# Optimization experiments

Measured on AMD Instinct MI355X. Metric: run time of the kernel, lower is better.

## Reference

```python
import jax, jax.numpy as jnp
import numpy as np

N_NODES = 100_000
N_EDGES = 3_200_000
N_FEAT = 128
HIDDEN = 16
OUT = 2
N_GRAPHS = 64


def setup_inputs() -> dict:
    key = jax.random.key(0)
    ks = jax.random.split(key, 12)
    x = jax.random.normal(ks[0], (N_NODES, N_FEAT), dtype=jnp.float32)
    edge_index = jax.random.randint(ks[1], (2, N_EDGES), 0, N_NODES, dtype=jnp.int64)
    batch_idx = jnp.sort(jax.random.randint(ks[2], (N_NODES,), 0, N_GRAPHS, dtype=jnp.int64))

    def glorot(k, shape):
        s = jnp.sqrt(6.0 / (shape[0] + shape[1])).astype(jnp.float32)
        return jax.random.uniform(k, shape, jnp.float32, -1.0, 1.0) * s

    return {
        "x": x, "edge_index": edge_index, "batch_idx": batch_idx,
        "W0": glorot(ks[3], (N_FEAT, HIDDEN)), "b0": jnp.zeros((HIDDEN,), jnp.float32),
        "a0": jnp.full((1,), 0.25, jnp.float32),  # PReLU default weight
        "W1": glorot(ks[4], (HIDDEN, HIDDEN)), "b1": jnp.zeros((HIDDEN,), jnp.float32),
        "a1": jnp.full((1,), 0.25, jnp.float32),
        "W2": glorot(ks[5], (HIDDEN, HIDDEN)), "b2": jnp.zeros((HIDDEN,), jnp.float32),
        "a2": jnp.full((1,), 0.25, jnp.float32),
        "W3": glorot(ks[6], (HIDDEN, OUT)), "b3": jnp.zeros((OUT,), jnp.float32),
    }


def _prelu(x, a):
    return jnp.where(x > 0, x, a * x)


def _gcn_conv(x, W, b, src, dst, norm, n):
    # PyG GCNConv: linear transform, then normalized gather-scatter aggregation, then bias
    h = x @ W                                   # [N, out]
    msg = h[src] * norm[:, None]                # gather + per-edge scale
    out = jax.ops.segment_sum(msg, dst, num_segments=n)  # scatter-add into targets
    return out + b


def reference(x, edge_index, batch_idx, W0, b0, a0, W1, b1, a1, W2, b2, a2, W3, b3):
    n = x.shape[0]
    loop = jnp.arange(n, dtype=edge_index.dtype)
    src = jnp.concatenate([edge_index[0], loop])  # add self loops
    dst = jnp.concatenate([edge_index[1], loop])
    # symmetric degree normalization deg^-1/2 (deg over targets, all edge weights = 1)
    deg = jax.ops.segment_sum(jnp.ones_like(dst, dtype=x.dtype), dst, num_segments=n)
    dinv = jnp.where(deg > 0, jax.lax.rsqrt(deg), 0.0)
    norm = dinv[src] * dinv[dst]

    h = _prelu(_gcn_conv(x, W0, b0, src, dst, norm, n), a0)
    h = _prelu(_gcn_conv(h, W1, b1, src, dst, norm, n), a1)
    h = _prelu(_gcn_conv(h, W2, b2, src, dst, norm, n), a2)
    h = _gcn_conv(h, W3, b3, src, dst, norm, n)

    # global_mean_pool over graph ids
    sums = jax.ops.segment_sum(h, batch_idx, num_segments=N_GRAPHS)
    cnts = jax.ops.segment_sum(jnp.ones((n,), h.dtype), batch_idx, num_segments=N_GRAPHS)
    return sums / jnp.maximum(cnts, 1.0)[:, None]
```

## Files before the change

### kernel.cpp

```cpp
#include <hip/hip_runtime.h>


#define NN 100000
#define NE 3200000
#define NF 128
#define NH 16
#define NO 2
#define NG 64
#define NBLK 391
#define BN 256
#define NBUK 391
#define CHUNK 4096
#define NBLKA 782
#define CAP2 10240


__device__ __forceinline__ float ldf(const void* p, int i, int f32) {
  if (f32) return ((const float*)p)[i];
  unsigned int u = ((const unsigned short*)p)[i];
  return __uint_as_float(u << 16);
}
__device__ __forceinline__ int ldi(const void* p, int i, int i64) {
  if (i64) return (int)((const long long*)p)[i];
  return ((const int*)p)[i];
}
__device__ __forceinline__ void stf(void* p, int i, float v, int f32) {
  if (f32) {
    ((float*)p)[i] = v;
  } else {
    unsigned int w = __float_as_uint(v);
    unsigned int r = (w + 0x7fffu + ((w >> 16) & 1u)) >> 16;
    ((unsigned short*)p)[i] = (unsigned short)r;
  }
}
__device__ __forceinline__ float bf16lo(unsigned int u) { return __uint_as_float(u << 16); }
__device__ __forceinline__ float bf16hi(unsigned int u) { return __uint_as_float(u & 0xffff0000u); }
__device__ __forceinline__ unsigned int packbf(float x, float y) {
  unsigned int a = __float_as_uint(x);
  a = (a + 0x7fffu + ((a >> 16) & 1u)) >> 16;
  unsigned int b = __float_as_uint(y);
  b = (b + 0x7fffu + ((b >> 16) & 1u)) & 0xffff0000u;
  return a | b;
}
__device__ __forceinline__ int okf(float v) { return (v == v) && (fabsf(v) < 1e30f); }
__device__ __forceinline__ void nflag(int* diag, int bad, int bit) {
  if (__any(bad)) {
    if ((threadIdx.x & 63) == 0) atomicOr(diag + 2, 1 << bit);
  }
}
__device__ __forceinline__ int clampi(int v, int hi) {
  return (unsigned)v < (unsigned)hi ? v : 0;
}


__global__ __launch_bounds__(64) void k_sniff(const void* x, const void* ei, int* diag) {
  int lane = threadIdx.x;
  unsigned int xv = ((const unsigned int*)x)[lane];
  unsigned int e = (xv >> 7) & 0xffu;
  int hit = (e >= 116u && e <= 133u);
  int hits = __popcll(__ballot(hit));
  unsigned int ev = ((const unsigned int*)ei)[2 * lane + 1];
  int nzc = __popcll(__ballot(ev != 0u));
  if (lane == 0) {
    diag[0] = (hits < 32) ? 1 : 0;
    diag[1] = (nzc == 0) ? 1 : 0;
  }
}


__global__ __launch_bounds__(256) void k_count(const void* ei, const int* __restrict__ diag,
                                               int* __restrict__ matrix) {
  __shared__ int lh[NBUK];
  int tid = threadIdx.x, blk = blockIdx.x;
  for (int b = tid; b < NBUK; b += 256) lh[b] = 0;
  __syncthreads();
  int i64 = diag[1];
  int base = blk * CHUNK;
  int n = NE - base; n = n > CHUNK ? CHUNK : n;
  for (int i = tid; i < n; i += 256) {
    int d = clampi(ldi(ei, NE + base + i, i64), NN);
    atomicAdd(&lh[d >> 8], 1);
  }
  __syncthreads();
  for (int b = tid; b < NBUK; b += 256) matrix[blk * NBUK + b] = lh[b];
}

__global__ __launch_bounds__(256) void k_rowscan(int* __restrict__ matrix, int* __restrict__ bucket_start) {
  __shared__ int s[1024];
  int tid = threadIdx.x, b = blockIdx.x;
#pragma unroll
  for (int k = 0; k < 4; ++k) {
    int i = tid + 256 * k;
    s[i] = (i < NBLKA) ? matrix[i * NBUK + b] : 0;
  }
  __syncthreads();
  for (int off = 1; off < 1024; off <<= 1) {
    int v[4];
#pragma unroll
    for (int k = 0; k < 4; ++k) { int i = tid + 256 * k; v[k] = (i >= off) ? s[i - off] : 0; }
    __syncthreads();
#pragma unroll
    for (int k = 0; k < 4; ++k) s[tid + 256 * k] += v[k];
    __syncthreads();
  }
#pragma unroll
  for (int k = 0; k < 4; ++k) {
    int i = tid + 256 * k;
    if (i < NBLKA) matrix[i * NBUK + b] = (i > 0) ? s[i - 1] : 0;
  }
  if (tid == 0) bucket_start[b] = s[1023];
}

__global__ __launch_bounds__(512) void k_sscan(int* __restrict__ bucket_start, int* __restrict__ rowstart) {
  __shared__ int s[512];
  int tid = threadIdx.x;
  int v = (tid < NBUK) ? bucket_start[tid] : 0;
  s[tid] = v;
  __syncthreads();
  for (int off = 1; off < 512; off <<= 1) {
    int t = (tid >= off) ? s[tid - off] : 0;
    __syncthreads();
    s[tid] += t;
    __syncthreads();
  }
  if (tid < NBUK) bucket_start[tid] = s[tid] - v;
  if (tid == 511) bucket_start[NBUK] = s[511];
  if (tid == 0) rowstart[NN] = NE;
}

__global__ __launch_bounds__(256) void k_bscatter(const void* ei, const int* __restrict__ diag,
                                                  const int* __restrict__ matrix,
                                                  const int* __restrict__ bucket_start,
                                                  int* __restrict__ ents) {
  __shared__ int ssrc[CHUNK];
  __shared__ int sdst[CHUNK];
  __shared__ int spkt[CHUNK];
  __shared__ int gpos[CHUNK];
  __shared__ int lhist[512];
  __shared__ int lcur[NBUK];
  __shared__ int goff[NBUK];
  int tid = threadIdx.x, blk = blockIdx.x;
  lhist[tid] = 0; lhist[tid + 256] = 0;
  __syncthreads();
  int i64 = diag[1];
  int base = blk * CHUNK;
  int n = NE - base; n = n > CHUNK ? CHUNK : n;
  for (int i = tid; i < n; i += 256) {
    int sv = clampi(ldi(ei, base + i, i64), NN);
    int dv = clampi(ldi(ei, NE + base + i, i64), NN);
    ssrc[i] = sv; sdst[i] = dv;
    atomicAdd(&lhist[dv >> 8], 1);
  }
  __syncthreads();
  for (int off = 1; off < 512; off <<= 1) {
    int v0 = (tid >= off) ? lhist[tid - off] : 0;
    int v1 = lhist[tid + 256 - off];
    __syncthreads();
    lhist[tid] += v0;
    lhist[tid + 256] += v1;
    __syncthreads();
  }
  for (int b = tid; b < NBUK; b += 256) {
    int excl = (b > 0) ? lhist[b - 1] : 0;
    lcur[b] = excl;
    goff[b] = bucket_start[b] + matrix[blk * NBUK + b] - excl;
  }
  __syncthreads();
  for (int i = tid; i < n; i += 256) {
    int dv = sdst[i], b = dv >> 8;
    int r = atomicAdd(&lcur[b], 1);
    spkt[r] = ((dv & 255) << 17) | ssrc[i];
    gpos[r] = goff[b] + r;
  }
  __syncthreads();
  for (int i = tid; i < n; i += 256) ents[gpos[i]] = spkt[i];
}

__global__ __launch_bounds__(256) void k_bsort(int* __restrict__ ents, const int* __restrict__ bucket_start,
                                               int* __restrict__ rowstart, float* __restrict__ dinv,
                                               int* __restrict__ diag) {
  __shared__ int ent[CAP2];
  __shared__ int lh[BN];
  __shared__ int lcur[BN];
  int tid = threadIdx.x, b = blockIdx.x;
  int bs = bucket_start[b], be = bucket_start[b + 1];
  int n = be - bs;
  if (n > CAP2) { n = CAP2; if (tid == 0) atomicOr(diag + 2, 1 << 9); }
  for (int i = tid; i < n; i += 256) ent[i] = ents[bs + i];
  lh[tid] = 0;
  __syncthreads();
  for (int i = tid; i < n; i += 256) atomicAdd(&lh[ent[i] >> 17], 1);
  __syncthreads();
  int c = lh[tid];
  for (int off = 1; off < 256; off <<= 1) {
    int v = (tid >= off) ? lh[tid - off] : 0;
    __syncthreads();
    lh[tid] += v;
    __syncthreads();
  }
  int excl = lh[tid] - c;
  lcur[tid] = excl;
  int node = (b << 8) + tid;
  if (node < NN) {
    rowstart[node] = bs + excl;
    dinv[node] = rsqrtf((float)(c + 1));
  }
  __syncthreads();
  for (int i = tid; i < n; i += 256) {
    int e = ent[i];
    int r = atomicAdd(&lcur[e >> 17], 1);
    ents[bs + r] = e & 0x1FFFF;
  }
}


__global__ __launch_bounds__(256) void k_t0(const void* __restrict__ x, const void* __restrict__ W0,
                                            const float* __restrict__ dinv,
                                            int* __restrict__ diag, unsigned int* __restrict__ out) {
  __shared__ float ws[NF * NH];
  __shared__ float xs[16 * 129];
  int tid = threadIdx.x;
  int f32 = diag[0];
  int node0 = blockIdx.x * 16;
#pragma unroll
  for (int r = 0; r < 8; ++r) ws[tid + 256 * r] = ldf(W0, tid + 256 * r, f32);
#pragma unroll
  for (int r = 0; r < 8; ++r) {
    int idx = tid + 256 * r;
    int row = idx >> 7, col = idx & 127;
    xs[row * 129 + col] = ldf(x, (node0 + row) * NF + col, f32);
  }
  __syncthreads();
  int nl = tid >> 4, f = tid & 15;
  float acc = 0.f;
#pragma unroll 4
  for (int k = 0; k < NF; ++k) acc += xs[nl * 129 + k] * ws[k * NH + f];
  acc *= dinv[node0 + nl];
  float other = __shfl_xor(acc, 1);
  if ((f & 1) == 0) out[(node0 + nl) * 8 + (f >> 1)] = packbf(acc, other);
  nflag(diag, !okf(acc), 0);
}


__global__ __launch_bounds__(256) void k_aggT(const unsigned int* __restrict__ hin,
                                              const int* __restrict__ srcs,
                                              const int* __restrict__ rowstart,
                                              const float* __restrict__ dinv,
                                              const void* __restrict__ b, const void* __restrict__ a,
                                              const void* __restrict__ Wn,
                                              int* __restrict__ diag, int bit,
                                              unsigned int* __restrict__ hout) {
  __shared__ float ws[NH * NH];
  int tid = threadIdx.x;
  int f32 = diag[0];
  ws[tid] = ldf(Wn, tid, f32);
  __syncthreads();
  int gid = blockIdx.x * 256 + tid;
  int node = gid >> 3, p = gid & 7;
  unsigned int self = hin[node * 8 + p];
  float acc0 = bf16lo(self), acc1 = bf16hi(self);
  int e0 = rowstart[node], e1 = rowstart[node + 1];
  int e = e0;
  for (; e + 4 <= e1; e += 4) {
    int s0 = srcs[e], s1 = srcs[e + 1], s2 = srcs[e + 2], s3 = srcs[e + 3];
    unsigned int v0 = hin[s0 * 8 + p];
    unsigned int v1 = hin[s1 * 8 + p];
    unsigned int v2 = hin[s2 * 8 + p];
    unsigned int v3 = hin[s3 * 8 + p];
    acc0 += bf16lo(v0) + bf16lo(v1) + bf16lo(v2) + bf16lo(v3);
    acc1 += bf16hi(v0) + bf16hi(v1) + bf16hi(v2) + bf16hi(v3);
  }
  for (; e < e1; ++e) {
    unsigned int v = hin[srcs[e] * 8 + p];
    acc0 += bf16lo(v);
    acc1 += bf16hi(v);
  }
  float dv = dinv[node];
  float av = ldf(a, 0, f32);
  float p0 = dv * acc0 + ldf(b, 2 * p, f32);
  float p1 = dv * acc1 + ldf(b, 2 * p + 1, f32);
  p0 = p0 > 0.f ? p0 : av * p0;
  p1 = p1 > 0.f ? p1 : av * p1;
  float t0 = 0.f, t1 = 0.f;
#pragma unroll
  for (int j = 0; j < 8; ++j) {
    float qa = __shfl(p0, j, 8);
    float qb = __shfl(p1, j, 8);
    t0 += qa * ws[(2 * j) * NH + 2 * p]     + qb * ws[(2 * j + 1) * NH + 2 * p];
    t1 += qa * ws[(2 * j) * NH + 2 * p + 1] + qb * ws[(2 * j + 1) * NH + 2 * p + 1];
  }
  t0 *= dv;
  t1 *= dv;
  hout[node * 8 + p] = packbf(t0, t1);
  nflag(diag, !okf(t0) || !okf(t1), bit);
}

__global__ __launch_bounds__(256) void k_aggT3(const unsigned int* __restrict__ hin,
                                               const int* __restrict__ srcs,
                                               const int* __restrict__ rowstart,
                                               const float* __restrict__ dinv,
                                               const void* __restrict__ b, const void* __restrict__ a,
                                               const void* __restrict__ W3,
                                               int* __restrict__ diag, float2* __restrict__ hout) {
  __shared__ float ws[NH * NO];
  int tid = threadIdx.x;
  int f32 = diag[0];
  if (tid < NH * NO) ws[tid] = ldf(W3, tid, f32);
  __syncthreads();
  int gid = blockIdx.x * 256 + tid;
  int node = gid >> 3, p = gid & 7;
  unsigned int self = hin[node * 8 + p];
  float acc0 = bf16lo(self), acc1 = bf16hi(self);
  int e0 = rowstart[node], e1 = rowstart[node + 1];
  int e = e0;
  for (; e + 4 <= e1; e += 4) {
    int s0 = srcs[e], s1 = srcs[e + 1], s2 = srcs[e + 2], s3 = srcs[e + 3];
    unsigned int v0 = hin[s0 * 8 + p];
    unsigned int v1 = hin[s1 * 8 + p];
    unsigned int v2 = hin[s2 * 8 + p];
    unsigned int v3 = hin[s3 * 8 + p];
    acc0 += bf16lo(v0) + bf16lo(v1) + bf16lo(v2) + bf16lo(v3);
    acc1 += bf16hi(v0) + bf16hi(v1) + bf16hi(v2) + bf16hi(v3);
  }
  for (; e < e1; ++e) {
    unsigned int v = hin[srcs[e] * 8 + p];
    acc0 += bf16lo(v);
    acc1 += bf16hi(v);
  }
  float dv = dinv[node];
  float av = ldf(a, 0, f32);
  float p0 = dv * acc0 + ldf(b, 2 * p, f32);
  float p1 = dv * acc1 + ldf(b, 2 * p + 1, f32);
  p0 = p0 > 0.f ? p0 : av * p0;
  p1 = p1 > 0.f ? p1 : av * p1;
  float u0 = p0 * ws[(2 * p) * NO] + p1 * ws[(2 * p + 1) * NO];
  float u1 = p0 * ws[(2 * p) * NO + 1] + p1 * ws[(2 * p + 1) * NO + 1];
#pragma unroll
  for (int off = 1; off < 8; off <<= 1) {
    u0 += __shfl_xor(u0, off, 8);
    u1 += __shfl_xor(u1, off, 8);
  }
  if (p == 0) hout[node] = make_float2(dv * u0, dv * u1);
  nflag(diag, !okf(u0) || !okf(u1), 6);
}

__global__ __launch_bounds__(256) void k_agg2(const float2* __restrict__ tin,
                                              const int* __restrict__ srcs,
                                              const int* __restrict__ rowstart,
                                              const float* __restrict__ dinv,
                                              const void* __restrict__ b3,
                                              int* __restrict__ diag, float2* __restrict__ out) {
  int node = blockIdx.x * 256 + threadIdx.x;
  if (node >= NN) return;
  int f32 = diag[0];
  float2 t = tin[node];
  float a0 = t.x, a1 = t.y;
  int e0 = rowstart[node], e1 = rowstart[node + 1];
  int e = e0;
  for (; e + 4 <= e1; e += 4) {
    int s0 = srcs[e], s1 = srcs[e + 1], s2 = srcs[e + 2], s3 = srcs[e + 3];
    float2 h0 = tin[s0], h1 = tin[s1], h2 = tin[s2], h3 = tin[s3];
    a0 += h0.x + h1.x + h2.x + h3.x;
    a1 += h0.y + h1.y + h2.y + h3.y;
  }
  for (; e < e1; ++e) {
    float2 hv = tin[srcs[e]];
    a0 += hv.x;
    a1 += hv.y;
  }
  float dv = dinv[node];
  a0 = dv * a0 + ldf(b3, 0, f32);
  a1 = dv * a1 + ldf(b3, 1, f32);
  out[node] = make_float2(a0, a1);
  nflag(diag, !okf(a0) || !okf(a1), 7);
}


__global__ __launch_bounds__(256) void k_pool(const float2* __restrict__ h, const void* __restrict__ batch,
                                              const int* __restrict__ diag, float* __restrict__ pool) {
  __shared__ float ssum[NG * NO];
  __shared__ float scnt[NG];
  int tid = threadIdx.x;
  if (tid < NG * NO) ssum[tid] = 0.f;
  if (tid < NG) scnt[tid] = 0.f;
  __syncthreads();
  int i = blockIdx.x * 256 + tid;
  if (i < NN) {
    int i64 = diag[1];
    int g = ldi(batch, i, i64);
    g = (unsigned)g < NG ? g : 0;
    float2 v = h[i];
    atomicAdd(&ssum[g * 2], v.x);
    atomicAdd(&ssum[g * 2 + 1], v.y);
    atomicAdd(&scnt[g], 1.f);
  }
  __syncthreads();
  if (tid < NG * NO && ssum[tid] != 0.f) atomicAdd(&pool[tid], ssum[tid]);
  if (tid < NG && scnt[tid] != 0.f) atomicAdd(&pool[NG * NO + tid], scnt[tid]);
}

__global__ __launch_bounds__(128) void k_final(const float* __restrict__ pool,
                                               const int* __restrict__ diag, void* __restrict__ out) {
  int i = threadIdx.x;
  int f32 = diag[0], i64 = diag[1], stg = diag[2];
  float c = pool[NG * NO + (i >> 1)];
  c = c > 1.f ? c : 1.f;
  float v = pool[i] / c;
  if (stg != 0 || !okf(v)) {
    int stage = stg ? __ffs(stg) : 15;
    v = 1024.0f + stage * 64.0f + f32 * 16.0f + i64 * 8.0f;
  }
  stf(out, i, v, f32);
}

__global__ __launch_bounds__(128) void k_diag_ws(void* out, float v) {
  unsigned int w = __float_as_uint(v);
  ((unsigned short*)out)[threadIdx.x] = (unsigned short)(w >> 16);
}


extern "C" void kernel_launch(void* const* d_in, const int* in_sizes, int n_in,
                              void* d_out, int out_size, void* d_ws, size_t ws_size,
                              hipStream_t stream) {
  const void* x  = d_in[0];
  const void* ei = d_in[1];
  const void* batch = d_in[2];
  const void* W0 = d_in[3];
  const void* b0 = d_in[4];
  const void* a0 = d_in[5];
  const void* W1 = d_in[6];
  const void* b1 = d_in[7];
  const void* a1 = d_in[8];
  const void* W2 = d_in[9];
  const void* b2 = d_in[10];
  const void* a2 = d_in[11];
  const void* W3 = d_in[12];
  const void* b3 = d_in[13];

  char* w = (char*)d_ws;
  int* diag         = (int*)(w + 0);
  float* pool       = (float*)(w + 64);
  float* dinv       = (float*)(w + 896);
  int* rowstart     = (int*)(w + 400960);
  int* bucket_start = (int*)(w + 801088);
  int* ents         = (int*)(w + 804288);
  unsigned int* hsA = (unsigned int*)(w + 13604288);
  unsigned int* hsB = (unsigned int*)(w + 16804288);
  float2* hs3       = (float2*)(w + 20004288);
  float2* out2      = (float2*)(w + 20804288);
  int* matrix       = (int*)hsA;
  const size_t NEED = 21604288;

  if (ws_size < NEED) {
    k_diag_ws<<<1, 128, 0, stream>>>(d_out, (float)ws_size);
    return;
  }

  hipMemsetAsync(d_ws, 0, 832, stream);

  k_sniff<<<1, 64, 0, stream>>>(x, ei, diag);

  k_count<<<NBLKA, 256, 0, stream>>>(ei, diag, matrix);
  k_rowscan<<<NBUK, 256, 0, stream>>>(matrix, bucket_start);
  k_sscan<<<1, 512, 0, stream>>>(bucket_start, rowstart);
  k_bscatter<<<NBLKA, 256, 0, stream>>>(ei, diag, matrix, bucket_start, ents);
  k_bsort<<<NBUK, 256, 0, stream>>>(ents, bucket_start, rowstart, dinv, diag);

  k_t0<<<NN / 16, 256, 0, stream>>>(x, W0, dinv, diag, hsA);
  k_aggT<<<NN * 8 / 256, 256, 0, stream>>>(hsA, ents, rowstart, dinv, b0, a0, W1, diag, 1, hsB);
  k_aggT<<<NN * 8 / 256, 256, 0, stream>>>(hsB, ents, rowstart, dinv, b1, a1, W2, diag, 3, hsA);
  k_aggT3<<<NN * 8 / 256, 256, 0, stream>>>(hsA, ents, rowstart, dinv, b2, a2, W3, diag, hs3);
  k_agg2<<<NBLK, 256, 0, stream>>>(hs3, ents, rowstart, dinv, b3, diag, out2);

  k_pool<<<NBLK, 256, 0, stream>>>(out2, batch, diag, pool);
  k_final<<<1, 128, 0, stream>>>(pool, diag, d_out);
}
```

Before: 332.3 us.

## Build CSR in fixed-capacity buckets via atomic cursors; use MFMA for first layer

Replaces the count/rowscan/sscan/scatter pipeline with a single build kernel that reserves space in fixed-capacity per-bucket regions using global atomic cursors, so a rowend array replaces contiguous rowstart. This removes three kernel launches and a full extra pass over the destination indices. The first-layer transform also switches to bf16 MFMA 16x16x32 when the inputs are bf16, with four tiles per block. Risks are wasted padding in the edge array and overflow being clamped if a bucket exceeds its capacity.

New measurement: 318.5 us. 1.04x faster.

```diff
diff --git a/kernel.cpp b/kernel.cpp
--- a/kernel.cpp
+++ b/kernel.cpp
@@ -12,7 +12,11 @@
 #define NBUK 391
 #define CHUNK 4096
 #define NBLKA 782
-#define CAP2 10240
+#define CAPF 10240
+#define NT0 6250
+
+typedef __attribute__((ext_vector_type(8))) short short8;
+typedef __attribute__((ext_vector_type(4))) float float4v;
 
 
 __device__ __forceinline__ float ldf(const void* p, int i, int f32) {
@@ -68,70 +72,8 @@
 }
 
 
-__global__ __launch_bounds__(256) void k_count(const void* ei, const int* __restrict__ diag,
-                                               int* __restrict__ matrix) {
-  __shared__ int lh[NBUK];
-  int tid = threadIdx.x, blk = blockIdx.x;
-  for (int b = tid; b < NBUK; b += 256) lh[b] = 0;
-  __syncthreads();
-  int i64 = diag[1];
-  int base = blk * CHUNK;
-  int n = NE - base; n = n > CHUNK ? CHUNK : n;
-  for (int i = tid; i < n; i += 256) {
-    int d = clampi(ldi(ei, NE + base + i, i64), NN);
-    atomicAdd(&lh[d >> 8], 1);
-  }
-  __syncthreads();
-  for (int b = tid; b < NBUK; b += 256) matrix[blk * NBUK + b] = lh[b];
-}
-
-__global__ __launch_bounds__(256) void k_rowscan(int* __restrict__ matrix, int* __restrict__ bucket_start) {
-  __shared__ int s[1024];
-  int tid = threadIdx.x, b = blockIdx.x;
-#pragma unroll
-  for (int k = 0; k < 4; ++k) {
-    int i = tid + 256 * k;
-    s[i] = (i < NBLKA) ? matrix[i * NBUK + b] : 0;
-  }
-  __syncthreads();
-  for (int off = 1; off < 1024; off <<= 1) {
-    int v[4];
-#pragma unroll
-    for (int k = 0; k < 4; ++k) { int i = tid + 256 * k; v[k] = (i >= off) ? s[i - off] : 0; }
-    __syncthreads();
-#pragma unroll
-    for (int k = 0; k < 4; ++k) s[tid + 256 * k] += v[k];
-    __syncthreads();
-  }
-#pragma unroll
-  for (int k = 0; k < 4; ++k) {
-    int i = tid + 256 * k;
-    if (i < NBLKA) matrix[i * NBUK + b] = (i > 0) ? s[i - 1] : 0;
-  }
-  if (tid == 0) bucket_start[b] = s[1023];
-}
-
-__global__ __launch_bounds__(512) void k_sscan(int* __restrict__ bucket_start, int* __restrict__ rowstart) {
-  __shared__ int s[512];
-  int tid = threadIdx.x;
-  int v = (tid < NBUK) ? bucket_start[tid] : 0;
-  s[tid] = v;
-  __syncthreads();
-  for (int off = 1; off < 512; off <<= 1) {
-    int t = (tid >= off) ? s[tid - off] : 0;
-    __syncthreads();
-    s[tid] += t;
-    __syncthreads();
-  }
-  if (tid < NBUK) bucket_start[tid] = s[tid] - v;
-  if (tid == 511) bucket_start[NBUK] = s[511];
-  if (tid == 0) rowstart[NN] = NE;
-}
-
-__global__ __launch_bounds__(256) void k_bscatter(const void* ei, const int* __restrict__ diag,
-                                                  const int* __restrict__ matrix,
-                                                  const int* __restrict__ bucket_start,
-                                                  int* __restrict__ ents) {
+__global__ __launch_bounds__(256) void k_build(const void* ei, const int* __restrict__ diag,
+                                               int* __restrict__ cursor, int* __restrict__ ents) {
   __shared__ int ssrc[CHUNK];
   __shared__ int sdst[CHUNK];
   __shared__ int spkt[CHUNK];
@@ -161,31 +103,36 @@
     __syncthreads();
   }
   for (int b = tid; b < NBUK; b += 256) {
+    int incl = lhist[b];
     int excl = (b > 0) ? lhist[b - 1] : 0;
+    int cnt = incl - excl;
     lcur[b] = excl;
-    goff[b] = bucket_start[b] + matrix[blk * NBUK + b] - excl;
+    int rbase = cnt ? atomicAdd(&cursor[b], cnt) : 0;
+    goff[b] = b * CAPF + rbase - excl;
   }
   __syncthreads();
   for (int i = tid; i < n; i += 256) {
     int dv = sdst[i], b = dv >> 8;
     int r = atomicAdd(&lcur[b], 1);
     spkt[r] = ((dv & 255) << 17) | ssrc[i];
-    gpos[r] = goff[b] + r;
+    int gp = goff[b] + r;
+    int hi = b * CAPF + CAPF - 1;
+    gpos[r] = gp <= hi ? gp : hi;
   }
   __syncthreads();
   for (int i = tid; i < n; i += 256) ents[gpos[i]] = spkt[i];
 }
 
-__global__ __launch_bounds__(256) void k_bsort(int* __restrict__ ents, const int* __restrict__ bucket_start,
-                                               int* __restrict__ rowstart, float* __restrict__ dinv,
-                                               int* __restrict__ diag) {
-  __shared__ int ent[CAP2];
+__global__ __launch_bounds__(256) void k_bsort(int* __restrict__ ents, const int* __restrict__ cursor,
+                                               int* __restrict__ rowstart, int* __restrict__ rowend,
+                                               float* __restrict__ dinv, int* __restrict__ diag) {
+  __shared__ int ent[CAPF];
   __shared__ int lh[BN];
   __shared__ int lcur[BN];
   int tid = threadIdx.x, b = blockIdx.x;
-  int bs = bucket_start[b], be = bucket_start[b + 1];
-  int n = be - bs;
-  if (n > CAP2) { n = CAP2; if (tid == 0) atomicOr(diag + 2, 1 << 9); }
+  int bs = b * CAPF;
+  int n = cursor[b];
+  if (n > CAPF) { n = CAPF; if (tid == 0) atomicOr(diag + 2, 1 << 9); }
   for (int i = tid; i < n; i += 256) ent[i] = ents[bs + i];
   lh[tid] = 0;
   __syncthreads();
@@ -203,6 +150,7 @@
   int node = (b << 8) + tid;
   if (node < NN) {
     rowstart[node] = bs + excl;
+    rowend[node] = bs + excl + c;
     dinv[node] = rsqrtf((float)(c + 1));
   }
   __syncthreads();
@@ -221,30 +169,72 @@
   __shared__ float xs[16 * 129];
   int tid = threadIdx.x;
   int f32 = diag[0];
-  int node0 = blockIdx.x * 16;
-#pragma unroll
-  for (int r = 0; r < 8; ++r) ws[tid + 256 * r] = ldf(W0, tid + 256 * r, f32);
-#pragma unroll
-  for (int r = 0; r < 8; ++r) {
-    int idx = tid + 256 * r;
-    int row = idx >> 7, col = idx & 127;
-    xs[row * 129 + col] = ldf(x, (node0 + row) * NF + col, f32);
-  }
-  __syncthreads();
-  int nl = tid >> 4, f = tid & 15;
-  float acc = 0.f;
+  if (!f32) {
+    const unsigned short* xu = (const unsigned short*)x;
+    const unsigned short* wu = (const unsigned short*)W0;
+    int wave = tid >> 6, lane = tid & 63;
+    int nfe = lane & 15, quad = lane >> 4;
+    short8 bfr[4];
+#pragma unroll
+    for (int mf = 0; mf < 4; ++mf) {
+      short8 t;
+#pragma unroll
+      for (int j = 0; j < 8; ++j) t[j] = (short)wu[(mf * 32 + quad * 8 + j) * NH + nfe];
+      bfr[mf] = t;
+    }
+    int tile = blockIdx.x * 4 + wave;
+    if (tile < NT0) {
+      int node0 = tile * 16;
+      const short8* xrow = (const short8*)(xu + (node0 + nfe) * NF);
+      float4v c = {0.f, 0.f, 0.f, 0.f};
+#pragma unroll
+      for (int mf = 0; mf < 4; ++mf) {
+        short8 a = xrow[mf * 4 + quad];
+        c = __builtin_amdgcn_mfma_f32_16x16x32_bf16(a, bfr[mf], c, 0, 0, 0);
+      }
+      int bad = 0;
+#pragma unroll
+      for (int r = 0; r < 4; ++r) {
+        int node = node0 + quad * 4 + r;
+        float v = c[r] * dinv[node];
+        float o = __shfl_xor(v, 1);
+        if (!(nfe & 1)) out[node * 8 + (nfe >> 1)] = packbf(v, o);
+        bad |= !okf(v);
+      }
+      nflag(diag, bad, 0);
+    }
+  } else {
+    for (int t = 0; t < 4; ++t) {
+      int tile = blockIdx.x * 4 + t;
+      if (tile >= NT0) break;
+      int node0 = tile * 16;
+      __syncthreads();
+#pragma unroll
+      for (int r = 0; r < 8; ++r) ws[tid + 256 * r] = ldf(W0, tid + 256 * r, 1);
+#pragma unroll
+      for (int r = 0; r < 8; ++r) {
+        int idx = tid + 256 * r;
+        int row = idx >> 7, col = idx & 127;
+        xs[row * 129 + col] = ldf(x, (node0 + row) * NF + col, 1);
+      }
+      __syncthreads();
+      int nl = tid >> 4, f = tid & 15;
+      float acc = 0.f;
 #pragma unroll 4
-  for (int k = 0; k < NF; ++k) acc += xs[nl * 129 + k] * ws[k * NH + f];
-  acc *= dinv[node0 + nl];
-  float other = __shfl_xor(acc, 1);
-  if ((f & 1) == 0) out[(node0 + nl) * 8 + (f >> 1)] = packbf(acc, other);
-  nflag(diag, !okf(acc), 0);
+      for (int k = 0; k < NF; ++k) acc += xs[nl * 129 + k] * ws[k * NH + f];
+      acc *= dinv[node0 + nl];
+      float other = __shfl_xor(acc, 1);
+      if ((f & 1) == 0) out[(node0 + nl) * 8 + (f >> 1)] = packbf(acc, other);
+      nflag(diag, !okf(acc), 0);
+    }
+  }
 }
 
 
 __global__ __launch_bounds__(256) void k_aggT(const unsigned int* __restrict__ hin,
                                               const int* __restrict__ srcs,
                                               const int* __restrict__ rowstart,
+                                              const int* __restrict__ rowend,
                                               const float* __restrict__ dinv,
                                               const void* __restrict__ b, const void* __restrict__ a,
                                               const void* __restrict__ Wn,
@@ -259,8 +249,7 @@
   int node = gid >> 3, p = gid & 7;
   unsigned int self = hin[node * 8 + p];
   float acc0 = bf16lo(self), acc1 = bf16hi(self);
-  int e0 = rowstart[node], e1 = rowstart[node + 1];
-  int e = e0;
+  int e = rowstart[node], e1 = rowend[node];
   for (; e + 4 <= e1; e += 4) {
     int s0 = srcs[e], s1 = srcs[e + 1], s2 = srcs[e + 2], s3 = srcs[e + 3];
     unsigned int v0 = hin[s0 * 8 + p];
@@ -298,6 +287,7 @@
 __global__ __launch_bounds__(256) void k_aggT3(const unsigned int* __restrict__ hin,
                                                const int* __restrict__ srcs,
                                                const int* __restrict__ rowstart,
+                                               const int* __restrict__ rowend,
                                                const float* __restrict__ dinv,
                                                const void* __restrict__ b, const void* __restrict__ a,
                                                const void* __restrict__ W3,
@@ -311,8 +301,7 @@
   int node = gid >> 3, p = gid & 7;
   unsigned int self = hin[node * 8 + p];
   float acc0 = bf16lo(self), acc1 = bf16hi(self);
-  int e0 = rowstart[node], e1 = rowstart[node + 1];
-  int e = e0;
+  int e = rowstart[node], e1 = rowend[node];
   for (; e + 4 <= e1; e += 4) {
     int s0 = srcs[e], s1 = srcs[e + 1], s2 = srcs[e + 2], s3 = srcs[e + 3];
     unsigned int v0 = hin[s0 * 8 + p];
@@ -347,6 +336,7 @@
 __global__ __launch_bounds__(256) void k_agg2(const float2* __restrict__ tin,
                                               const int* __restrict__ srcs,
                                               const int* __restrict__ rowstart,
+                                              const int* __restrict__ rowend,
                                               const float* __restrict__ dinv,
                                               const void* __restrict__ b3,
                                               int* __restrict__ diag, float2* __restrict__ out) {
@@ -355,8 +345,7 @@
   int f32 = diag[0];
   float2 t = tin[node];
   float a0 = t.x, a1 = t.y;
-  int e0 = rowstart[node], e1 = rowstart[node + 1];
-  int e = e0;
+  int e = rowstart[node], e1 = rowend[node];
   for (; e + 4 <= e1; e += 4) {
     int s0 = srcs[e], s1 = srcs[e + 1], s2 = srcs[e + 2], s3 = srcs[e + 3];
     float2 h0 = tin[s0], h1 = tin[s1], h2 = tin[s2], h3 = tin[s3];
@@ -440,37 +429,34 @@
   char* w = (char*)d_ws;
   int* diag         = (int*)(w + 0);
   float* pool       = (float*)(w + 64);
-  float* dinv       = (float*)(w + 896);
-  int* rowstart     = (int*)(w + 400960);
-  int* bucket_start = (int*)(w + 801088);
-  int* ents         = (int*)(w + 804288);
-  unsigned int* hsA = (unsigned int*)(w + 13604288);
-  unsigned int* hsB = (unsigned int*)(w + 16804288);
-  float2* hs3       = (float2*)(w + 20004288);
-  float2* out2      = (float2*)(w + 20804288);
-  int* matrix       = (int*)hsA;
-  const size_t NEED = 21604288;
+  int* cursor       = (int*)(w + 896);
+  float* dinv       = (float*)(w + 2496);
+  int* rowstart     = (int*)(w + 402496);
+  int* rowend       = (int*)(w + 802496);
+  int* ents         = (int*)(w + 1202496);
+  unsigned int* hsA = (unsigned int*)(w + 17217856);
+  unsigned int* hsB = (unsigned int*)(w + 20417856);
+  float2* hs3       = (float2*)(w + 23617856);
+  float2* out2      = (float2*)(w + 24417856);
+  const size_t NEED = 25217856;
 
   if (ws_size < NEED) {
     k_diag_ws<<<1, 128, 0, stream>>>(d_out, (float)ws_size);
     return;
   }
 
-  hipMemsetAsync(d_ws, 0, 832, stream);
+  hipMemsetAsync(d_ws, 0, 2496, stream);
 
   k_sniff<<<1, 64, 0, stream>>>(x, ei, diag);
 
-  k_count<<<NBLKA, 256, 0, stream>>>(ei, diag, matrix);
-  k_rowscan<<<NBUK, 256, 0, stream>>>(matrix, bucket_start);
-  k_sscan<<<1, 512, 0, stream>>>(bucket_start, rowstart);
-  k_bscatter<<<NBLKA, 256, 0, stream>>>(ei, diag, matrix, bucket_start, ents);
-  k_bsort<<<NBUK, 256, 0, stream>>>(ents, bucket_start, rowstart, dinv, diag);
-
-  k_t0<<<NN / 16, 256, 0, stream>>>(x, W0, dinv, diag, hsA);
-  k_aggT<<<NN * 8 / 256, 256, 0, stream>>>(hsA, ents, rowstart, dinv, b0, a0, W1, diag, 1, hsB);
-  k_aggT<<<NN * 8 / 256, 256, 0, stream>>>(hsB, ents, rowstart, dinv, b1, a1, W2, diag, 3, hsA);
-  k_aggT3<<<NN * 8 / 256, 256, 0, stream>>>(hsA, ents, rowstart, dinv, b2, a2, W3, diag, hs3);
-  k_agg2<<<NBLK, 256, 0, stream>>>(hs3, ents, rowstart, dinv, b3, diag, out2);
+  k_build<<<NBLKA, 256, 0, stream>>>(ei, diag, cursor, ents);
+  k_bsort<<<NBUK, 256, 0, stream>>>(ents, cursor, rowstart, rowend, dinv, diag);
+
+  k_t0<<<(NT0 + 3) / 4, 256, 0, stream>>>(x, W0, dinv, diag, hsA);
+  k_aggT<<<NN * 8 / 256, 256, 0, stream>>>(hsA, ents, rowstart, rowend, dinv, b0, a0, W1, diag, 1, hsB);
+  k_aggT<<<NN * 8 / 256, 256, 0, stream>>>(hsB, ents, rowstart, rowend, dinv, b1, a1, W2, diag, 3, hsA);
+  k_aggT3<<<NN * 8 / 256, 256, 0, stream>>>(hsA, ents, rowstart, rowend, dinv, b2, a2, W3, diag, hs3);
+  k_agg2<<<NBLK, 256, 0, stream>>>(hs3, ents, rowstart, rowend, dinv, b3, diag, out2);
 
   k_pool<<<NBLK, 256, 0, stream>>>(out2, batch, diag, pool);
   k_final<<<1, 128, 0, stream>>>(pool, diag, d_out);
```
